# Optimization experiments

Hardware: AMD Instinct MI355X
Metric: run time of the kernel (lower is better)

The kernel has to match this reference:

```python
import jax, jax.numpy as jnp
import numpy as np

NUM_NODES = 512

def chebyshev_convolution(laplacian, signal, weights, t0):
    # Faithful port of the torch helper, including tk_prev staying equal to
    # `laplacian` throughout the loop (as in the source).
    k = weights.shape[0]
    # t0 is the identity, so t0 @ signal == signal
    out = jnp.matmul(signal, weights[0])
    out = out + jnp.matmul(jnp.matmul(laplacian, signal), weights[1])
    tk_prev = laplacian
    tk = 2.0 * jnp.matmul(laplacian, laplacian) - t0
    for i in range(2, k):
        out = out + jnp.matmul(jnp.matmul(tk, signal), weights[i])
        tk = 2.0 * jnp.matmul(laplacian, tk) - tk_prev
    return out


def setup_inputs() -> dict:
    key = jax.random.key(0)
    ks = jax.random.split(key, 5)
    B, T, N, C_IN, C_OUT, CS, CD = 4, 12, NUM_NODES, 64, 64, 3, 6
    std_l = 0.1 / np.sqrt(N)
    std_t = 0.1 / np.sqrt(C_IN)
    x = jax.random.normal(ks[0], (B, T, N, C_IN), dtype=jnp.float32)
    ws = jax.random.uniform(ks[1], (N, N), jnp.float32, -std_l, std_l)
    ts = jax.random.uniform(ks[2], (CS, C_IN, C_OUT), jnp.float32, -std_t, std_t)
    wp = jax.random.uniform(ks[3], (C_IN, C_IN), jnp.float32, -std_t, std_t)
    td = jax.random.uniform(ks[4], (CD, C_IN, C_OUT), jnp.float32, -std_t, std_t)
    return {"x": x, "ws": ws, "ts": ts, "wp": wp, "td": td}


def reference(x, ws, ts, wp, td):
    N = NUM_NODES
    t0 = jnp.eye(N, dtype=x.dtype)
    # Static (SGC) branch: Chebyshev conv with learned static Laplacian ws
    out_s = chebyshev_convolution(ws, x, ts, t0)
    # Dynamic branch: data-dependent Laplacian wd = x @ (wp @ x^T)  -> (B,T,N,N)
    wd = jnp.matmul(x, jnp.matmul(wp, jnp.swapaxes(x, -2, -1)))
    wd = wd + jnp.min(wd)
    wd = wd / jnp.max(wd) / (N ** 2)
    out_d = chebyshev_convolution(wd, x, td, t0)
    return out_s + out_d
```

## Files before the change

### kernel.cpp

```cpp
#include <hip/hip_runtime.h>
#include <cstddef>
#include <cstdint>

#define NN 512
#define CC 64
#define BT 48

typedef __bf16 bf16_t;
typedef bf16_t bf16x8 __attribute__((ext_vector_type(8)));
typedef bf16_t bf16x4 __attribute__((ext_vector_type(4)));
typedef float f32x4 __attribute__((ext_vector_type(4)));

#define OFF_MN    0
#define OFF_MX    384
#define OFF_WSB   1024
#define OFF_WS2B  132096
#define OFF_XBT   263168
#define OFF_XNB   1049600
#define OFF_XNR   1836032
#define OFF_CS0   2622464
#define OFF_T1T   2647040
#define OFF_T2T   2649088

__device__ __forceinline__ f32x4 mfma(bf16x8 a, bf16x8 b, f32x4 c) {
  return __builtin_amdgcn_mfma_f32_16x16x32_bf16(a, b, c, 0, 0, 0);
}
__device__ __forceinline__ int swz_chunk(int r, int c8) {
  return r * 64 + ((c8 ^ (r & 7)) << 3);
}
__device__ __forceinline__ int swz_e(int r, int c) {
  return r * 64 + ((((c >> 3) ^ (r & 7)) << 3)) + (c & 7);
}
__device__ __forceinline__ bf16x8 frag(const bf16_t* sm, int row, int kc) {
  return *(const bf16x8*)(sm + row * 64 + ((kc ^ (row & 7)) << 3));
}
__device__ __forceinline__ void stage64(bf16_t* sm, const bf16_t* g, int ld, int tid) {
#pragma unroll
  for (int j = 0; j < 2; ++j) {
    int id = tid + 256 * j;
    int r = id >> 3, c8 = id & 7;
    bf16x8 v = *(const bf16x8*)(g + (size_t)r * ld + c8 * 8);
    *(bf16x8*)(sm + swz_chunk(r, c8)) = v;
  }
}
__device__ __forceinline__ void stage64f(bf16_t* sm, const float* g, int ld, int tid) {
#pragma unroll
  for (int j = 0; j < 4; ++j) {
    int idx = tid + 256 * j;
    int r = idx >> 4, cc = (idx & 15) * 4;
    float4 v = *(const float4*)(g + (size_t)r * ld + cc);
    bf16x4 o = {(bf16_t)v.x, (bf16_t)v.y, (bf16_t)v.z, (bf16_t)v.w};
    *(bf16x4*)(sm + swz_e(r, cc)) = o;
  }
}
struct bfpair { bf16_t b, r; };
__device__ __forceinline__ bfpair splitbf(float f) {
  bfpair p;
  p.b = (bf16_t)f;
  p.r = (bf16_t)(f - (float)p.b);
  return p;
}

__global__ __launch_bounds__(256) void k_pre(
    const float* __restrict__ x, const float* __restrict__ wsL,
    const float* __restrict__ ts, const float* __restrict__ wp,
    float* __restrict__ wsf)
{
  __shared__ __align__(16) char pool[32768];
  __shared__ float red[16];
  const int tid = threadIdx.x;
  const int b = blockIdx.x;
  const int w = tid >> 6, l = tid & 63, lh = l >> 4, lr = l & 15, m0 = w * 16;

  if (b < 384) {
    const int bt = (b & 7) + 8 * (b >> 6);
    const int it = (b >> 3) & 7;
    const int i0 = it * 64;
    float (*XsF)[66] = (float(*)[66])pool;
    bf16_t* XBT = (bf16_t*)(wsf + OFF_XBT);
    bf16_t* XNb = (bf16_t*)(wsf + OFF_XNB);
    bf16_t* XNr = (bf16_t*)(wsf + OFF_XNR);
    float* CS0 = wsf + OFF_CS0;
    const float* xg = x + ((size_t)bt * NN + i0) * CC;
    for (int j = 0; j < 4; ++j) {
      int idx = tid + 256 * j;
      int r = idx >> 4, c0v = (idx & 15) * 4;
      float4 v = *(const float4*)(xg + (size_t)r * CC + c0v);
      bfpair p0 = splitbf(v.x), p1 = splitbf(v.y), p2 = splitbf(v.z), p3 = splitbf(v.w);
      bf16x4 vb = {p0.b, p1.b, p2.b, p3.b};
      bf16x4 vr = {p0.r, p1.r, p2.r, p3.r};
      size_t gb = ((size_t)bt * 512 + i0 + r) * 64 + c0v;
      *(bf16x4*)(XNb + gb) = vb;
      *(bf16x4*)(XNr + gb) = vr;
      XsF[c0v + 0][r] = v.x; XsF[c0v + 1][r] = v.y;
      XsF[c0v + 2][r] = v.z; XsF[c0v + 3][r] = v.w;
    }
    __syncthreads();
    {
      int c = tid >> 2, k0 = (tid & 3) * 16;
      bf16x8 o1, o2;
#pragma unroll
      for (int q = 0; q < 8; ++q) {
        o1[q] = (bf16_t)XsF[c][k0 + q];
        o2[q] = (bf16_t)XsF[c][k0 + 8 + q];
      }
      size_t base = ((size_t)bt * 64 + c) * 512 + i0 + k0;
      *(bf16x8*)(XBT + base) = o1; *(bf16x8*)(XBT + base + 8) = o2;
    }
    if (tid < 64) {
      float s = 0.f;
      for (int r = 0; r < 64; ++r) s += XsF[tid][r];
      CS0[((size_t)bt * 8 + it) * 64 + tid] = s;
    }
    return;
  }
  if (b < 768) {
    const int g = b - 384;
    const int bt = (g & 7) + 8 * (g >> 6);
    const int bx = (g >> 3) & 7;
    bf16_t* WpT  = (bf16_t*)pool;
    bf16_t* Xa   = (bf16_t*)(pool + 8192);
    bf16_t* Hs   = (bf16_t*)(pool + 16384);
    bf16_t* Xcol = (bf16_t*)(pool + 24576);
    for (int j = 0; j < 4; ++j) {
      int idx = tid + 256 * j;
      int r = idx >> 4, cc = (idx & 15) * 4;
      float4 v = *(const float4*)(wp + r * 64 + cc);
      WpT[swz_e(cc + 0, r)] = (bf16_t)v.x;
      WpT[swz_e(cc + 1, r)] = (bf16_t)v.y;
      WpT[swz_e(cc + 2, r)] = (bf16_t)v.z;
      WpT[swz_e(cc + 3, r)] = (bf16_t)v.w;
    }
    stage64f(Xa, x + ((size_t)bt * NN + bx * 64) * CC, 64, tid);
    __syncthreads();
    f32x4 hacc[4] = {};
#pragma unroll
    for (int q = 0; q < 2; ++q) {
      bf16x8 a = frag(Xa, m0 + lr, q * 4 + lh);
#pragma unroll
      for (int t = 0; t < 4; ++t)
        hacc[t] = mfma(a, frag(WpT, t * 16 + lr, q * 4 + lh), hacc[t]);
    }
#pragma unroll
    for (int t = 0; t < 4; ++t)
#pragma unroll
      for (int r_ = 0; r_ < 4; ++r_)
        Hs[swz_e(m0 + 4 * lh + r_, t * 16 + lr)] = (bf16_t)hacc[t][r_];
    float mn = 3.4e38f, mx = -3.4e38f;
    for (int byj = 0; byj < 8; ++byj) {
      __syncthreads();
      stage64f(Xcol, x + ((size_t)bt * NN + byj * 64) * CC, 64, tid);
      __syncthreads();
      f32x4 acc[4] = {};
#pragma unroll
      for (int q = 0; q < 2; ++q) {
        bf16x8 a = frag(Hs, m0 + lr, q * 4 + lh);
#pragma unroll
        for (int t = 0; t < 4; ++t)
          acc[t] = mfma(a, frag(Xcol, t * 16 + lr, q * 4 + lh), acc[t]);
      }
#pragma unroll
      for (int t = 0; t < 4; ++t)
#pragma unroll
        for (int r_ = 0; r_ < 4; ++r_) {
          mn = fminf(mn, acc[t][r_]); mx = fmaxf(mx, acc[t][r_]);
        }
    }
    for (int off = 32; off; off >>= 1) {
      mn = fminf(mn, __shfl_xor(mn, off));
      mx = fmaxf(mx, __shfl_xor(mx, off));
    }
    if (l == 0) { red[w] = mn; red[8 + w] = mx; }
    __syncthreads();
    if (tid == 0) {
      mn = fminf(fminf(red[0], red[1]), fminf(red[2], red[3]));
      mx = fmaxf(fmaxf(red[8], red[9]), fmaxf(red[10], red[11]));
      wsf[OFF_MN + g] = mn; wsf[OFF_MX + g] = mx;
    }
    return;
  }
  if (b < 832) {
    const int idx2 = b - 768;
    bf16_t* Asb = (bf16_t*)pool;
    bf16_t* Bsb = (bf16_t*)(pool + 8192);
    bf16_t* Ys  = (bf16_t*)(pool + 16384);
    bf16_t* WS2B = (bf16_t*)(wsf + OFF_WS2B);
    const int r0 = (idx2 >> 3) * 64, c0 = (idx2 & 7) * 64;
    f32x4 acc[4] = {};
    for (int jj = 0; jj < 8; ++jj) {
      if (jj) __syncthreads();
      for (int j = 0; j < 4; ++j) {
        int idx = tid + 256 * j;
        int r = idx >> 4, cc = (idx & 15) * 4;
        float4 v = *(const float4*)(wsL + (size_t)(r0 + r) * 512 + jj * 64 + cc);
        bf16x4 vb = {(bf16_t)v.x, (bf16_t)v.y, (bf16_t)v.z, (bf16_t)v.w};
        *(bf16x4*)(Asb + swz_e(r, cc)) = vb;
        float4 u = *(const float4*)(wsL + (size_t)(jj * 64 + r) * 512 + c0 + cc);
        Bsb[swz_e(cc + 0, r)] = (bf16_t)u.x;
        Bsb[swz_e(cc + 1, r)] = (bf16_t)u.y;
        Bsb[swz_e(cc + 2, r)] = (bf16_t)u.z;
        Bsb[swz_e(cc + 3, r)] = (bf16_t)u.w;
      }
      __syncthreads();
#pragma unroll
      for (int q = 0; q < 2; ++q) {
        bf16x8 a = frag(Asb, m0 + lr, q * 4 + lh);
#pragma unroll
        for (int t = 0; t < 4; ++t)
          acc[t] = mfma(a, frag(Bsb, t * 16 + lr, q * 4 + lh), acc[t]);
      }
    }
#pragma unroll
    for (int t = 0; t < 4; ++t)
#pragma unroll
      for (int r_ = 0; r_ < 4; ++r_) {
        int row = m0 + 4 * lh + r_, col = t * 16 + lr;
        float v = 2.0f * acc[t][r_] - ((r0 + row) == (c0 + col) ? 1.0f : 0.0f);
        Ys[swz_e(row, col)] = (bf16_t)v;
      }
    __syncthreads();
#pragma unroll
    for (int j = 0; j < 2; ++j) {
      int id = tid + 256 * j;
      int r = id >> 3, c8 = id & 7;
      *(bf16x8*)(WS2B + (size_t)(r0 + r) * 512 + c0 + c8 * 8) =
          *(const bf16x8*)(Ys + swz_chunk(r, c8));
    }
    return;
  }
  if (b < 840) {
    const int bx = b - 832;
    const float* wrow = wsL + (size_t)bx * 64 * 512;
    bf16_t* wob = (bf16_t*)(wsf + OFF_WSB) + (size_t)bx * 64 * 512;
    for (int j = 0; j < 32; ++j) {
      int idx = tid + 256 * j;
      float4 v = *(const float4*)(wrow + (size_t)idx * 4);
      bf16x4 o = {(bf16_t)v.x, (bf16_t)v.y, (bf16_t)v.z, (bf16_t)v.w};
      *(bf16x4*)(wob + (size_t)idx * 4) = o;
    }
    return;
  }
  {
    bf16_t* T1 = (bf16_t*)(wsf + OFF_T1T);
    bf16_t* T2 = (bf16_t*)(wsf + OFF_T2T);
    const float* t1g = ts + 4096;
    const float* t2g = ts + 8192;
    for (int j = 0; j < 16; ++j) {
      int idx = tid + 256 * j;
      int cin = idx >> 6, co = idx & 63;
      T1[co * 64 + cin] = (bf16_t)t1g[cin * 64 + co];
      T2[co * 64 + cin] = (bf16_t)t2g[cin * 64 + co];
    }
  }
}

__global__ __launch_bounds__(256) void k_go(
    const float* __restrict__ ts, const float* __restrict__ wp,
    const float* __restrict__ td, float* __restrict__ wsf,
    float* __restrict__ out)
{
  __shared__ __align__(16) char pool[81920];
  const int tid = threadIdx.x;
  const int g = blockIdx.x;
  const int bt = (g & 7) + 8 * (g >> 6);
  const int n0 = ((g >> 3) & 7) * 64;
  const int w = tid >> 6, l = tid & 63, lh = l >> 4, lr = l & 15, m0 = w * 16;

  bf16_t* XB = (bf16_t*)pool;
  bf16_t* B1 = (bf16_t*)(pool + 65536);
  bf16_t* B2 = (bf16_t*)(pool + 73728);
  const bf16_t* XBTg = (const bf16_t*)(wsf + OFF_XBT);
  const bf16_t* WSB  = (const bf16_t*)(wsf + OFF_WSB);
  const bf16_t* WS2B = (const bf16_t*)(wsf + OFF_WS2B);
  for (int kk = 0; kk < 8; ++kk)
    stage64(XB + kk * 4096, XBTg + (size_t)bt * 32768 + kk * 64, 512, tid);
  f32x4 acc1[4] = {}, acc2[4] = {}, pacc[4] = {};
  for (int kk = 0; kk < 8; ++kk) {
    __syncthreads();
    stage64(B1, WSB + (size_t)n0 * 512 + kk * 64, 512, tid);
    stage64(B2, WS2B + (size_t)n0 * 512 + kk * 64, 512, tid);
    __syncthreads();
    const bf16_t* xt = XB + kk * 4096;
#pragma unroll
    for (int q = 0; q < 2; ++q) {
      bf16x8 a = frag(xt, m0 + lr, q * 4 + lh);
#pragma unroll
      for (int t = 0; t < 4; ++t) {
        acc1[t] = mfma(a, frag(B1, t * 16 + lr, q * 4 + lh), acc1[t]);
        acc2[t] = mfma(a, frag(B2, t * 16 + lr, q * 4 + lh), acc2[t]);
        pacc[t] = mfma(a, frag(xt, t * 16 + lr, q * 4 + lh), pacc[t]);
      }
    }
  }
  __syncthreads();

  bf16_t* Ab0 = (bf16_t*)pool;
  bf16_t* AT0 = (bf16_t*)(pool + 8192);
  bf16_t* Ab1 = (bf16_t*)(pool + 16384);
  bf16_t* AT1 = (bf16_t*)(pool + 24576);
  bf16_t* Gb  = (bf16_t*)(pool + 32768);
  bf16_t* WpT = (bf16_t*)(pool + 40960);
  bf16_t* WpN = (bf16_t*)(pool + 49152);
  bf16_t* tdA = (bf16_t*)(pool + 57344);
  bf16_t* tdB = (bf16_t*)(pool + 65536);
  float* vec = (float*)(pool + 73728);
  float* uF = vec;         float* hF = vec + 64;
  float* b0 = vec + 128;   float* b1 = vec + 192;
  float* vaccF = vec + 256;
  float* redv = vec + 320;
  const float* CS0 = wsf + OFF_CS0;
  {
    float mn = 3.4e38f, mx = -3.4e38f;
    for (int i = tid; i < 384; i += 256) {
      mn = fminf(mn, wsf[OFF_MN + i]);
      mx = fmaxf(mx, wsf[OFF_MX + i]);
    }
    for (int off = 32; off; off >>= 1) {
      mn = fminf(mn, __shfl_xor(mn, off));
      mx = fmaxf(mx, __shfl_xor(mx, off));
    }
    if (l == 0) { redv[w] = mn; redv[8 + w] = mx; }
  }
#pragma unroll
  for (int t = 0; t < 4; ++t)
#pragma unroll
    for (int r_ = 0; r_ < 4; ++r_) {
      int m = m0 + 4 * lh + r_, jc = t * 16 + lr;
      bf16_t bv = (bf16_t)pacc[t][r_];
      Ab0[swz_e(m, jc)] = bv; AT0[swz_e(jc, m)] = bv;
    }
  if (tid < 64) {
    float s = 0.f;
#pragma unroll
    for (int p = 0; p < 8; ++p) s += CS0[((size_t)bt * 8 + p) * 64 + tid];
    uF[tid] = s; b0[tid] = s; vaccF[tid] = 0.f;
  }
  for (int j = 0; j < 4; ++j) {
    int idx = tid + 256 * j;
    int r = idx >> 4, cc = (idx & 15) * 4;
    float4 v = *(const float4*)(wp + r * 64 + cc);
    bf16_t q0 = (bf16_t)v.x, q1 = (bf16_t)v.y, q2 = (bf16_t)v.z, q3 = (bf16_t)v.w;
    WpN[swz_e(r, cc + 0)] = q0; WpT[swz_e(cc + 0, r)] = q0;
    WpN[swz_e(r, cc + 1)] = q1; WpT[swz_e(cc + 1, r)] = q1;
    WpN[swz_e(r, cc + 2)] = q2; WpT[swz_e(cc + 2, r)] = q2;
    WpN[swz_e(r, cc + 3)] = q3; WpT[swz_e(cc + 3, r)] = q3;
  }
  for (int j = 0; j < 4; ++j) {
    int idx = tid + 256 * j;
    int cin = idx >> 4, co = (idx & 15) * 4;
    float4 v = *(const float4*)(td + 4096 + cin * 64 + co);
    tdA[swz_e(co + 0, cin)] = (bf16_t)v.x;
    tdA[swz_e(co + 1, cin)] = (bf16_t)v.y;
    tdA[swz_e(co + 2, cin)] = (bf16_t)v.z;
    tdA[swz_e(co + 3, cin)] = (bf16_t)v.w;
  }
  __syncthreads();
  const float mnA = fminf(fminf(redv[0], redv[1]), fminf(redv[2], redv[3]));
  const float mxA = fmaxf(fmaxf(redv[8], redv[9]), fmaxf(redv[10], redv[11]));
  const float s_sc = 1.0f / (mxA + mnA) / 262144.0f;
  const float c_sc = mnA * s_sc;
  {
    int jj = tid >> 2, sub = tid & 3;
    float s = 0.f;
    for (int c = sub * 16; c < sub * 16 + 16; ++c)
      s += (float)WpT[swz_e(jj, c)] * uF[c];
    s += __shfl_xor(s, 1); s += __shfl_xor(s, 2);
    if (sub == 0) hF[jj] = s;
  }
  {
    f32x4 gv[4] = {};
#pragma unroll
    for (int q = 0; q < 2; ++q) {
      bf16x8 a = frag(Ab0, m0 + lr, q * 4 + lh);
#pragma unroll
      for (int t = 0; t < 4; ++t)
        gv[t] = mfma(a, frag(WpT, t * 16 + lr, q * 4 + lh), gv[t]);
    }
#pragma unroll
    for (int t = 0; t < 4; ++t)
#pragma unroll
      for (int r_ = 0; r_ < 4; ++r_)
        Gb[swz_e(m0 + 4 * lh + r_, t * 16 + lr)] = (bf16_t)gv[t][r_];
  }
  __syncthreads();
  float mu = 0.f;
  f32x4 Macc[4] = {};
  for (int i = 1; i <= 5; ++i) {
    const float* bcur = (i & 1) ? b0 : b1;
    float* bnx = (i & 1) ? b1 : b0;
    const bf16_t* tdc = (i & 1) ? tdA : tdB;
    const bf16_t* AbC = (i & 1) ? Ab0 : Ab1;
    const bf16_t* ATC = (i & 1) ? AT0 : AT1;
    bf16_t* AbN = (i & 1) ? Ab1 : Ab0;
    bf16_t* ATN = (i & 1) ? AT1 : AT0;
    if (i < 5) {
      bf16_t* tdn = (i & 1) ? tdB : tdA;
      for (int j = 0; j < 4; ++j) {
        int idx = tid + 256 * j;
        int cin = idx >> 4, co = (idx & 15) * 4;
        float4 v = *(const float4*)(td + (i + 1) * 4096 + cin * 64 + co);
        tdn[swz_e(co + 0, cin)] = (bf16_t)v.x;
        tdn[swz_e(co + 1, cin)] = (bf16_t)v.y;
        tdn[swz_e(co + 2, cin)] = (bf16_t)v.z;
        tdn[swz_e(co + 3, cin)] = (bf16_t)v.w;
      }
    }
#pragma unroll
    for (int q = 0; q < 2; ++q) {
      bf16x8 a = frag(AbC, m0 + lr, q * 4 + lh);
#pragma unroll
      for (int t = 0; t < 4; ++t)
        Macc[t] = mfma(a, frag(tdc, t * 16 + lr, q * 4 + lh), Macc[t]);
    }
    f32x4 Aacc[4] = {};
    if (i < 5) {
#pragma unroll
      for (int q = 0; q < 2; ++q) {
        bf16x8 gfr = frag(Gb, m0 + lr, q * 4 + lh);
#pragma unroll
        for (int t = 0; t < 4; ++t)
          Aacc[t] = mfma(gfr, frag(ATC, t * 16 + lr, q * 4 + lh), Aacc[t]);
      }
    }
    {
      int co = tid >> 2, sub = tid & 3;
      float sv = 0.f;
      for (int c = sub * 16; c < sub * 16 + 16; ++c)
        sv += bcur[c] * (float)tdc[swz_e(co, c)];
      sv += __shfl_xor(sv, 1); sv += __shfl_xor(sv, 2);
      if (sub == 0) vaccF[co] += sv;
    }
    if (i < 5) {
      int jj = tid >> 2, sub = tid & 3;
      float t1 = 0.f;
      for (int m = sub * 16; m < sub * 16 + 16; ++m)
        t1 += (float)ATC[swz_e(jj, m)] * hF[m];
      t1 += __shfl_xor(t1, 1); t1 += __shfl_xor(t1, 2);
      if (sub == 0)
        bnx[jj] = 2.f * (s_sc * t1 + 512.f * c_sc * bcur[jj] + mu * uF[jj])
                  - (i >= 2 ? uF[jj] : 0.f);
    }
    if (i < 5) {
#pragma unroll
      for (int t = 0; t < 4; ++t)
#pragma unroll
        for (int r_ = 0; r_ < 4; ++r_) {
          int m = m0 + 4 * lh + r_, jc = t * 16 + lr;
          float v = 2.f * (s_sc * Aacc[t][r_] + c_sc * uF[m] * bcur[jc] + mu * pacc[t][r_])
                    - (i >= 2 ? pacc[t][r_] : 0.f);
          bf16_t bv = (bf16_t)v;
          AbN[swz_e(m, jc)] = bv; ATN[swz_e(jc, m)] = bv;
        }
      mu = (i == 1) ? -1.f : 0.f;
    }
    __syncthreads();
  }
  bf16_t* Mst = tdA;
#pragma unroll
  for (int t = 0; t < 4; ++t)
#pragma unroll
    for (int r_ = 0; r_ < 4; ++r_)
      Mst[swz_e(t * 16 + lr, m0 + 4 * lh + r_)] = (bf16_t)Macc[t][r_];
  __syncthreads();
  f32x4 wm[4] = {};
#pragma unroll
  for (int q = 0; q < 2; ++q) {
    bf16x8 a = frag(WpN, m0 + lr, q * 4 + lh);
#pragma unroll
    for (int t = 0; t < 4; ++t)
      wm[t] = mfma(a, frag(Mst, t * 16 + lr, q * 4 + lh), wm[t]);
  }
  __syncthreads();

  bf16_t* Z1s = (bf16_t*)pool;
  bf16_t* Z2s = (bf16_t*)(pool + 8192);
  bf16_t* Xb  = (bf16_t*)(pool + 16384);
  bf16_t* Xr  = (bf16_t*)(pool + 24576);
  bf16_t* WEs = (bf16_t*)(pool + 32768);
  bf16_t* WRs = (bf16_t*)(pool + 40960);
  bf16_t* T1s = (bf16_t*)(pool + 49152);
  bf16_t* T2s = (bf16_t*)(pool + 57344);
#pragma unroll
  for (int t = 0; t < 4; ++t)
#pragma unroll
    for (int r_ = 0; r_ < 4; ++r_) {
      int a_ = m0 + 4 * lh + r_, co = t * 16 + lr;
      float weff = ts[a_ * 64 + co] + td[a_ * 64 + co] - td[2 * 4096 + a_ * 64 + co]
                   + s_sc * wm[t][r_];
      bfpair p = splitbf(weff);
      WEs[swz_e(co, a_)] = p.b;
      WRs[swz_e(co, a_)] = p.r;
      int cy = a_, nl = co;
      Z1s[swz_e(nl, cy)] = (bf16_t)acc1[t][r_];
      Z2s[swz_e(nl, cy)] = (bf16_t)acc2[t][r_];
    }
  stage64(Xb,  (const bf16_t*)(wsf + OFF_XNB) + ((size_t)bt * 512 + n0) * 64, 64, tid);
  stage64(Xr,  (const bf16_t*)(wsf + OFF_XNR) + ((size_t)bt * 512 + n0) * 64, 64, tid);
  stage64(T1s, (const bf16_t*)(wsf + OFF_T1T), 64, tid);
  stage64(T2s, (const bf16_t*)(wsf + OFF_T2T), 64, tid);
  __syncthreads();
  f32x4 accO[4];
#pragma unroll
  for (int t = 0; t < 4; ++t) {
    float vv = c_sc * vaccF[t * 16 + lr];
    accO[t] = {vv, vv, vv, vv};
  }
#pragma unroll
  for (int q = 0; q < 2; ++q) {
    bf16x8 aXb = frag(Xb, m0 + lr, q * 4 + lh);
    bf16x8 aXr = frag(Xr, m0 + lr, q * 4 + lh);
    bf16x8 aZ1 = frag(Z1s, m0 + lr, q * 4 + lh);
    bf16x8 aZ2 = frag(Z2s, m0 + lr, q * 4 + lh);
#pragma unroll
    for (int t = 0; t < 4; ++t) {
      bf16x8 bWb = frag(WEs, t * 16 + lr, q * 4 + lh);
      bf16x8 bWr = frag(WRs, t * 16 + lr, q * 4 + lh);
      accO[t] = mfma(aXb, bWb, accO[t]);
      accO[t] = mfma(aXb, bWr, accO[t]);
      accO[t] = mfma(aXr, bWb, accO[t]);
      accO[t] = mfma(aZ1, frag(T1s, t * 16 + lr, q * 4 + lh), accO[t]);
      accO[t] = mfma(aZ2, frag(T2s, t * 16 + lr, q * 4 + lh), accO[t]);
    }
  }
#pragma unroll
  for (int t = 0; t < 4; ++t)
#pragma unroll
    for (int r_ = 0; r_ < 4; ++r_)
      out[((size_t)bt * 512 + n0 + m0 + 4 * lh + r_) * 64 + t * 16 + lr] = accO[t][r_];
}

extern "C" void kernel_launch(void* const* d_in, const int* in_sizes, int n_in,
                              void* d_out, int out_size, void* d_ws, size_t ws_size,
                              hipStream_t stream)
{
  (void)in_sizes; (void)n_in; (void)out_size; (void)ws_size;
  const float* x   = (const float*)d_in[0];
  const float* wsL = (const float*)d_in[1];
  const float* ts  = (const float*)d_in[2];
  const float* wp  = (const float*)d_in[3];
  const float* td  = (const float*)d_in[4];
  float* out = (float*)d_out;
  float* wsf = (float*)d_ws;
  dim3 b(256);

  k_pre<<<841, b, 0, stream>>>(x, wsL, ts, wp, wsf);
  k_go <<<384, b, 0, stream>>>(ts, wp, td, wsf, out);
}
```

Baseline: 48.34 us.

## Split fused kernel into per-bt mixing kernel plus separate epilogue kernel

The old kernel recomputed the per-(b,t) dynamic Chebyshev recursion (the 64x64 Gram matrix and the five-step loop) redundantly in each of the 8 node-tile blocks. Now one block per bt does that chain once and 384 other blocks compute the Z1/Z2 projections, all within one 432-block launch. The results (Z1, Z2, effective weights, bias vector) are written to workspace, and a new epilogue kernel reads them back to form the output. This removes 8x redundant serial work and lowers LDS use, at the cost of an extra launch and global round trips for intermediates.

```diff
diff --git a/kernel.cpp b/kernel.cpp
--- a/kernel.cpp
+++ b/kernel.cpp
@@ -21,6 +21,11 @@
 #define OFF_CS0   2622464
 #define OFF_T1T   2647040
 #define OFF_T2T   2649088
+#define OFF_Z1N   2651136
+#define OFF_Z2N   3437568
+#define OFF_WEB   4224000
+#define OFF_WER   4322304
+#define OFF_VDY   4420608
 
 __device__ __forceinline__ f32x4 mfma(bf16x8 a, bf16x8 b, f32x4 c) {
   return __builtin_amdgcn_mfma_f32_16x16x32_bf16(a, b, c, 0, 0, 0);
@@ -254,61 +259,82 @@
   }
 }
 
-__global__ __launch_bounds__(256) void k_go(
+__global__ __launch_bounds__(256) void k_mix(
     const float* __restrict__ ts, const float* __restrict__ wp,
-    const float* __restrict__ td, float* __restrict__ wsf,
-    float* __restrict__ out)
+    const float* __restrict__ td, float* __restrict__ wsf)
 {
-  __shared__ __align__(16) char pool[81920];
+  __shared__ __align__(16) char pool[66688];
   const int tid = threadIdx.x;
-  const int g = blockIdx.x;
-  const int bt = (g & 7) + 8 * (g >> 6);
-  const int n0 = ((g >> 3) & 7) * 64;
+  const int bid = blockIdx.x;
   const int w = tid >> 6, l = tid & 63, lh = l >> 4, lr = l & 15, m0 = w * 16;
 
-  bf16_t* XB = (bf16_t*)pool;
-  bf16_t* B1 = (bf16_t*)(pool + 65536);
-  bf16_t* B2 = (bf16_t*)(pool + 73728);
-  const bf16_t* XBTg = (const bf16_t*)(wsf + OFF_XBT);
-  const bf16_t* WSB  = (const bf16_t*)(wsf + OFF_WSB);
-  const bf16_t* WS2B = (const bf16_t*)(wsf + OFF_WS2B);
-  for (int kk = 0; kk < 8; ++kk)
-    stage64(XB + kk * 4096, XBTg + (size_t)bt * 32768 + kk * 64, 512, tid);
-  f32x4 acc1[4] = {}, acc2[4] = {}, pacc[4] = {};
-  for (int kk = 0; kk < 8; ++kk) {
+  if (bid >= 48) {
+    const int g = bid - 48;
+    const int bt = (g & 7) + 8 * (g >> 6);
+    const int n0 = ((g >> 3) & 7) * 64;
+    bf16_t* As = (bf16_t*)pool;
+    bf16_t* B1 = (bf16_t*)(pool + 8192);
+    bf16_t* B2 = (bf16_t*)(pool + 16384);
+    const bf16_t* XBT = (const bf16_t*)(wsf + OFF_XBT);
+    const bf16_t* WSB = (const bf16_t*)(wsf + OFF_WSB);
+    const bf16_t* WS2B = (const bf16_t*)(wsf + OFF_WS2B);
+    f32x4 acc1[4] = {}, acc2[4] = {};
+    for (int kk = 0; kk < 8; ++kk) {
+      if (kk) __syncthreads();
+      stage64(As, XBT + (size_t)bt * 32768 + kk * 64, 512, tid);
+      stage64(B1, WSB + (size_t)n0 * 512 + kk * 64, 512, tid);
+      stage64(B2, WS2B + (size_t)n0 * 512 + kk * 64, 512, tid);
+      __syncthreads();
+#pragma unroll
+      for (int q = 0; q < 2; ++q) {
+        bf16x8 a = frag(As, m0 + lr, q * 4 + lh);
+#pragma unroll
+        for (int t = 0; t < 4; ++t) {
+          acc1[t] = mfma(a, frag(B1, t * 16 + lr, q * 4 + lh), acc1[t]);
+          acc2[t] = mfma(a, frag(B2, t * 16 + lr, q * 4 + lh), acc2[t]);
+        }
+      }
+    }
     __syncthreads();
-    stage64(B1, WSB + (size_t)n0 * 512 + kk * 64, 512, tid);
-    stage64(B2, WS2B + (size_t)n0 * 512 + kk * 64, 512, tid);
+#pragma unroll
+    for (int t = 0; t < 4; ++t)
+#pragma unroll
+      for (int r_ = 0; r_ < 4; ++r_) {
+        int cy = m0 + 4 * lh + r_, nl = t * 16 + lr;
+        As[swz_e(nl, cy)] = (bf16_t)acc1[t][r_];
+        B1[swz_e(nl, cy)] = (bf16_t)acc2[t][r_];
+      }
     __syncthreads();
-    const bf16_t* xt = XB + kk * 4096;
-#pragma unroll
-    for (int q = 0; q < 2; ++q) {
-      bf16x8 a = frag(xt, m0 + lr, q * 4 + lh);
-#pragma unroll
-      for (int t = 0; t < 4; ++t) {
-        acc1[t] = mfma(a, frag(B1, t * 16 + lr, q * 4 + lh), acc1[t]);
-        acc2[t] = mfma(a, frag(B2, t * 16 + lr, q * 4 + lh), acc2[t]);
-        pacc[t] = mfma(a, frag(xt, t * 16 + lr, q * 4 + lh), pacc[t]);
-      }
-    }
-  }
-  __syncthreads();
-
+    bf16_t* Z1N = (bf16_t*)(wsf + OFF_Z1N);
+    bf16_t* Z2N = (bf16_t*)(wsf + OFF_Z2N);
+#pragma unroll
+    for (int j = 0; j < 2; ++j) {
+      int id = tid + 256 * j;
+      int r = id >> 3, c8 = id & 7;
+      size_t gb = ((size_t)bt * 512 + n0 + r) * 64 + c8 * 8;
+      *(bf16x8*)(Z1N + gb) = *(const bf16x8*)(As + swz_chunk(r, c8));
+      *(bf16x8*)(Z2N + gb) = *(const bf16x8*)(B1 + swz_chunk(r, c8));
+    }
+    return;
+  }
+  const int bt = bid;
+  bf16_t* XB  = (bf16_t*)pool;
   bf16_t* Ab0 = (bf16_t*)pool;
   bf16_t* AT0 = (bf16_t*)(pool + 8192);
   bf16_t* Ab1 = (bf16_t*)(pool + 16384);
   bf16_t* AT1 = (bf16_t*)(pool + 24576);
   bf16_t* Gb  = (bf16_t*)(pool + 32768);
   bf16_t* WpT = (bf16_t*)(pool + 40960);
-  bf16_t* WpN = (bf16_t*)(pool + 49152);
-  bf16_t* tdA = (bf16_t*)(pool + 57344);
-  bf16_t* tdB = (bf16_t*)(pool + 65536);
-  float* vec = (float*)(pool + 73728);
-  float* uF = vec;         float* hF = vec + 64;
-  float* b0 = vec + 128;   float* b1 = vec + 192;
-  float* vaccF = vec + 256;
-  float* redv = vec + 320;
+  bf16_t* tdA = (bf16_t*)(pool + 49152);
+  bf16_t* tdB = (bf16_t*)(pool + 57344);
+  float* vec = (float*)(pool + 65536);
+  float* uF = vec;        float* hF = vec + 64;
+  float* b0 = vec + 128;  float* b1 = vec + 192;
+  float* redv = vec + 256;
+  const bf16_t* XBTg = (const bf16_t*)(wsf + OFF_XBT);
   const float* CS0 = wsf + OFF_CS0;
+  for (int kk = 0; kk < 8; ++kk)
+    stage64(XB + kk * 4096, XBTg + (size_t)bt * 32768 + kk * 64, 512, tid);
   {
     float mn = 3.4e38f, mx = -3.4e38f;
     for (int i = tid; i < 384; i += 256) {
@@ -321,6 +347,29 @@
     }
     if (l == 0) { redv[w] = mn; redv[8 + w] = mx; }
   }
+  if (tid < 64) {
+    float s = 0.f;
+#pragma unroll
+    for (int p = 0; p < 8; ++p) s += CS0[((size_t)bt * 8 + p) * 64 + tid];
+    uF[tid] = s; b0[tid] = s;
+  }
+  __syncthreads();
+  f32x4 pacc[4] = {};
+  for (int kk = 0; kk < 8; ++kk) {
+    const bf16_t* xt = XB + kk * 4096;
+#pragma unroll
+    for (int q = 0; q < 2; ++q) {
+      bf16x8 a = frag(xt, m0 + lr, q * 4 + lh);
+#pragma unroll
+      for (int t = 0; t < 4; ++t)
+        pacc[t] = mfma(a, frag(xt, t * 16 + lr, q * 4 + lh), pacc[t]);
+    }
+  }
+  const float mnA = fminf(fminf(redv[0], redv[1]), fminf(redv[2], redv[3]));
+  const float mxA = fmaxf(fmaxf(redv[8], redv[9]), fmaxf(redv[10], redv[11]));
+  const float s_sc = 1.0f / (mxA + mnA) / 262144.0f;
+  const float c_sc = mnA * s_sc;
+  __syncthreads();
 #pragma unroll
   for (int t = 0; t < 4; ++t)
 #pragma unroll
@@ -329,21 +378,14 @@
       bf16_t bv = (bf16_t)pacc[t][r_];
       Ab0[swz_e(m, jc)] = bv; AT0[swz_e(jc, m)] = bv;
     }
-  if (tid < 64) {
-    float s = 0.f;
-#pragma unroll
-    for (int p = 0; p < 8; ++p) s += CS0[((size_t)bt * 8 + p) * 64 + tid];
-    uF[tid] = s; b0[tid] = s; vaccF[tid] = 0.f;
-  }
   for (int j = 0; j < 4; ++j) {
     int idx = tid + 256 * j;
     int r = idx >> 4, cc = (idx & 15) * 4;
     float4 v = *(const float4*)(wp + r * 64 + cc);
-    bf16_t q0 = (bf16_t)v.x, q1 = (bf16_t)v.y, q2 = (bf16_t)v.z, q3 = (bf16_t)v.w;
-    WpN[swz_e(r, cc + 0)] = q0; WpT[swz_e(cc + 0, r)] = q0;
-    WpN[swz_e(r, cc + 1)] = q1; WpT[swz_e(cc + 1, r)] = q1;
-    WpN[swz_e(r, cc + 2)] = q2; WpT[swz_e(cc + 2, r)] = q2;
-    WpN[swz_e(r, cc + 3)] = q3; WpT[swz_e(cc + 3, r)] = q3;
+    WpT[swz_e(cc + 0, r)] = (bf16_t)v.x;
+    WpT[swz_e(cc + 1, r)] = (bf16_t)v.y;
+    WpT[swz_e(cc + 2, r)] = (bf16_t)v.z;
+    WpT[swz_e(cc + 3, r)] = (bf16_t)v.w;
   }
   for (int j = 0; j < 4; ++j) {
     int idx = tid + 256 * j;
@@ -355,10 +397,6 @@
     tdA[swz_e(co + 3, cin)] = (bf16_t)v.w;
   }
   __syncthreads();
-  const float mnA = fminf(fminf(redv[0], redv[1]), fminf(redv[2], redv[3]));
-  const float mxA = fmaxf(fmaxf(redv[8], redv[9]), fmaxf(redv[10], redv[11]));
-  const float s_sc = 1.0f / (mxA + mnA) / 262144.0f;
-  const float c_sc = mnA * s_sc;
   {
     int jj = tid >> 2, sub = tid & 3;
     float s = 0.f;
@@ -383,7 +421,7 @@
         Gb[swz_e(m0 + 4 * lh + r_, t * 16 + lr)] = (bf16_t)gv[t][r_];
   }
   __syncthreads();
-  float mu = 0.f;
+  float mu = 0.f, vacc = 0.f;
   f32x4 Macc[4] = {};
   for (int i = 1; i <= 5; ++i) {
     const float* bcur = (i & 1) ? b0 : b1;
@@ -428,7 +466,7 @@
       for (int c = sub * 16; c < sub * 16 + 16; ++c)
         sv += bcur[c] * (float)tdc[swz_e(co, c)];
       sv += __shfl_xor(sv, 1); sv += __shfl_xor(sv, 2);
-      if (sub == 0) vaccF[co] += sv;
+      if (sub == 0) vacc += sv;
     }
     if (i < 5) {
       int jj = tid >> 2, sub = tid & 3;
@@ -456,11 +494,19 @@
     __syncthreads();
   }
   bf16_t* Mst = tdA;
+  bf16_t* WpN = tdB;
 #pragma unroll
   for (int t = 0; t < 4; ++t)
 #pragma unroll
     for (int r_ = 0; r_ < 4; ++r_)
       Mst[swz_e(t * 16 + lr, m0 + 4 * lh + r_)] = (bf16_t)Macc[t][r_];
+  for (int j = 0; j < 4; ++j) {
+    int idx = tid + 256 * j;
+    int r = idx >> 4, cc = (idx & 15) * 4;
+    float4 v = *(const float4*)(wp + r * 64 + cc);
+    bf16x4 o = {(bf16_t)v.x, (bf16_t)v.y, (bf16_t)v.z, (bf16_t)v.w};
+    *(bf16x4*)(WpN + swz_e(r, cc)) = o;
+  }
   __syncthreads();
   f32x4 wm[4] = {};
 #pragma unroll
@@ -470,16 +516,8 @@
     for (int t = 0; t < 4; ++t)
       wm[t] = mfma(a, frag(Mst, t * 16 + lr, q * 4 + lh), wm[t]);
   }
-  __syncthreads();
-
-  bf16_t* Z1s = (bf16_t*)pool;
-  bf16_t* Z2s = (bf16_t*)(pool + 8192);
-  bf16_t* Xb  = (bf16_t*)(pool + 16384);
-  bf16_t* Xr  = (bf16_t*)(pool + 24576);
-  bf16_t* WEs = (bf16_t*)(pool + 32768);
-  bf16_t* WRs = (bf16_t*)(pool + 40960);
-  bf16_t* T1s = (bf16_t*)(pool + 49152);
-  bf16_t* T2s = (bf16_t*)(pool + 57344);
+  bf16_t* WEb = (bf16_t*)(wsf + OFF_WEB);
+  bf16_t* WEr = (bf16_t*)(wsf + OFF_WER);
 #pragma unroll
   for (int t = 0; t < 4; ++t)
 #pragma unroll
@@ -488,21 +526,36 @@
       float weff = ts[a_ * 64 + co] + td[a_ * 64 + co] - td[2 * 4096 + a_ * 64 + co]
                    + s_sc * wm[t][r_];
       bfpair p = splitbf(weff);
-      WEs[swz_e(co, a_)] = p.b;
-      WRs[swz_e(co, a_)] = p.r;
-      int cy = a_, nl = co;
-      Z1s[swz_e(nl, cy)] = (bf16_t)acc1[t][r_];
-      Z2s[swz_e(nl, cy)] = (bf16_t)acc2[t][r_];
-    }
+      WEb[((size_t)bt * 64 + co) * 64 + a_] = p.b;
+      WEr[((size_t)bt * 64 + co) * 64 + a_] = p.r;
+    }
+  if ((tid & 3) == 0) (wsf + OFF_VDY)[bt * 64 + (tid >> 2)] = c_sc * vacc;
+}
+
+__global__ __launch_bounds__(256) void k_epi(float* __restrict__ wsf,
+                                             float* __restrict__ out)
+{
+  __shared__ __align__(16) bf16_t Xb[4096], Xr[4096], Z1s[4096], Z2s[4096],
+                                  WEs[4096], WRs[4096], T1s[4096], T2s[4096];
+  const int tid = threadIdx.x;
+  const int g = blockIdx.x;
+  const int bt = (g & 7) + 8 * (g >> 6);
+  const int n0 = ((g >> 3) & 7) * 64;
+  const int w = tid >> 6, l = tid & 63, lh = l >> 4, lr = l & 15, m0 = w * 16;
   stage64(Xb,  (const bf16_t*)(wsf + OFF_XNB) + ((size_t)bt * 512 + n0) * 64, 64, tid);
   stage64(Xr,  (const bf16_t*)(wsf + OFF_XNR) + ((size_t)bt * 512 + n0) * 64, 64, tid);
+  stage64(Z1s, (const bf16_t*)(wsf + OFF_Z1N) + ((size_t)bt * 512 + n0) * 64, 64, tid);
+  stage64(Z2s, (const bf16_t*)(wsf + OFF_Z2N) + ((size_t)bt * 512 + n0) * 64, 64, tid);
+  stage64(WEs, (const bf16_t*)(wsf + OFF_WEB) + (size_t)bt * 4096, 64, tid);
+  stage64(WRs, (const bf16_t*)(wsf + OFF_WER) + (size_t)bt * 4096, 64, tid);
   stage64(T1s, (const bf16_t*)(wsf + OFF_T1T), 64, tid);
   stage64(T2s, (const bf16_t*)(wsf + OFF_T2T), 64, tid);
   __syncthreads();
+  const float* VDY = wsf + OFF_VDY;
   f32x4 accO[4];
 #pragma unroll
   for (int t = 0; t < 4; ++t) {
-    float vv = c_sc * vaccF[t * 16 + lr];
+    float vv = VDY[bt * 64 + t * 16 + lr];
     accO[t] = {vv, vv, vv, vv};
   }
 #pragma unroll
@@ -544,5 +597,6 @@
   dim3 b(256);
 
   k_pre<<<841, b, 0, stream>>>(x, wsL, ts, wp, wsf);
-  k_go <<<384, b, 0, stream>>>(ts, wp, td, wsf, out);
-}
+  k_mix<<<432, b, 0, stream>>>(ts, wp, td, wsf);
+  k_epi<<<384, b, 0, stream>>>(wsf, out);
+}
```

New measurement: 44.19 us. 1.09x faster.
